# Kernel tuning notes

Measured on AMD Instinct MI355X. Metric: run time of the kernel, lower is better.

## Reference

```python
import jax, jax.numpy as jnp
import numpy as np

# 2x2 string of 4 cores at these (h, w) positions; ring bond topology.
POS = [(0, 0), (0, 1), (1, 0), (1, 1)]
MIN_H, MAX_H = 0, 1
MIN_W, MAX_W = 0, 1
STD = 0.9  # DumbNormalInitialization std


def setup_inputs() -> dict:
    key = jax.random.key(0)
    k1, k2 = jax.random.split(key)
    # channels: first dim = in_num_channels (2), each [B, H, W, in_quantum]
    channels = jax.random.normal(k1, (2, 8, 128, 128, 4), dtype=jnp.float32)
    # cores: [n_cores, out_quantum, bond_left, bond_right, in_q0, in_q1]
    cores = STD * jax.random.normal(k2, (4, 2, 8, 8, 4, 4), dtype=jnp.float32)
    return {"channels": channels, "cores": cores}


def reference(channels, cores):
    ch0, ch1 = channels[0], channels[1]  # each [B, H, W, Qin]
    inters = []
    for i in range(4):
        # First stage: contract core's in_quantum dims with both channels per pixel
        # -> [B, out_q, H, W, bond_l, bond_r]
        t = jnp.einsum('qlrij,bhwi,bhwj->bqhwlr', cores[i], ch0, ch1)
        h, w = POS[i]
        pad_top = MAX_H - MIN_H - (h - MIN_H)
        pad_bot = h - MIN_H
        pad_left = MAX_W - MIN_W - (w - MIN_W)
        pad_right = w - MIN_W
        # pad spatial dims with value 1.0 (multiplicative identity)
        t = jnp.pad(
            t,
            ((0, 0), (0, 0), (pad_top, pad_bot), (pad_left, pad_right), (0, 0), (0, 0)),
            constant_values=1.0,
        )
        inters.append(t)
    # Second stage: ring contraction over bond dims (i->j->k->l->i)
    out = jnp.einsum('bphwij,bqhwjk,brhwkl,bshwli->bhwpqrs', *inters)
    B, Hp, Wp = out.shape[:3]
    out = out.reshape(B, Hp, Wp, -1)  # merge out_quantum dims
    dh = MAX_H - MIN_H
    dw = MAX_W - MIN_W
    return out[:, dh:Hp - dh, dw:Wp - dw, :]
```

## Files before the change

kernel.cpp:

```cpp
#include <hip/hip_runtime.h>


typedef __fp16 h2 __attribute__((ext_vector_type(2)));
typedef __fp16 h4 __attribute__((ext_vector_type(4)));
typedef float  f4 __attribute__((ext_vector_type(4)));

#define NB 8
#define NH 128
#define NW 128
#define HO 127
#define WO 127
#define CH1_OFF (NB*NH*NW*4)
#define PXSTR 648
#define ZOFF  640
#define CDROW 68
#define CDSTR 544
#define SS    20

#define PIN() asm volatile("" ::: "memory")
#define PKRTZ(a, b) __builtin_amdgcn_cvt_pkrtz((a), (b))

__device__ __forceinline__ f4 mfma16(h4 a, h4 b, f4 c) {
  return __builtin_amdgcn_mfma_f32_16x16x16f16(a, b, c, 0, 0, 0);
}

__global__ __launch_bounds__(64, 3)
void convsbs_fused(const float* __restrict__ ch,
                   const float* __restrict__ cores,
                   float* __restrict__ out) {
  const int lane = threadIdx.x & 63;
  const int quad = lane >> 4;
  const int nn   = lane & 15;
  const int x8   = lane & 7;
  const f4 F4Z = {0.f, 0.f, 0.f, 0.f};

  __shared__ __align__(16) __fp16 tbuf[8 * PXSTR];
  __shared__ __align__(16) __fp16 cdb[4 * CDSTR];
  __shared__ __align__(16) float  sbuf[4 * SS];

  if (lane < 8) *(h4*)(tbuf + lane * PXSTR + ZOFF) = (h4){0, 0, 0, 0};
  PIN();

  __fp16* wrbase = tbuf + nn * PXSTR + quad * 4;
  const bool wr = (nn < 8);

  h4 wf[4][8];
#pragma unroll
  for (int c = 0; c < 4; ++c)
#pragma unroll
    for (int bi = 0; bi < 8; ++bi) {
      const int rowIdx = bi * 16 + nn;
      const int q  = rowIdx >> 6;
      const int ua = (rowIdx >> 3) & 7;
      const int ub = rowIdx & 7;
      const int l = (c & 1) ? ub : ua;
      const int r = (c & 1) ? ua : ub;
      const float4 wv = *(const float4*)(
          cores + ((((c * 2 + q) * 8 + l) * 8 + r) << 4) + quad * 4);
      h2 p0 = PKRTZ(wv.x, wv.y), p1 = PKRTZ(wv.z, wv.w);
      wf[c][bi] = (h4){p0[0], p0[1], p1[0], p1[1]};
    }

  const int hq = nn >> 3, hb = nn & 7;
  const int ctA = (quad < 2) ? ((2 + hq) * 80 + hb * 8 + quad * 4) : ZOFF;
  const int ctB = (quad < 2) ? ( hq      * 80 + hb * 8 + quad * 4) : ZOFF;
  const int dA  = (quad < 2) ? ((4 + hq) * 80 + hb * 8 + quad * 4) : ZOFF;
  const int dB  = (quad < 2) ? ((6 + hq) * 80 + hb * 8 + quad * 4) : ZOFF;
  const int ctW = (hq * 2 + (quad >> 1)) * CDROW + hb * 8 + (quad & 1) * 4;
  const int dW  = (4 + (quad >> 1) * 2 + hq) * CDROW + hb * 8 + (quad & 1) * 4;
  const int eA  = (nn >> 2) * CDSTR + (nn & 3) * CDROW + quad * 4;
  const int eB  = (nn >> 2) * CDSTR + (4 + (nn & 3)) * CDROW + quad * 4;
  const bool sW = ((nn >> 2) == quad);
  const int sWo = quad * SS + (nn & 3) * 4;
  const int sRo = quad * SS + (nn & 3) * 4 + (nn >> 2);

  const int blk = blockIdx.x;
  const int by  = blk >> 2;
  const int b   = by / 127;
  const int y   = by - b * 127;
  const int xq  = (blk & 3) * 32;
  const float* rowbase = ch + (size_t)((b * NH + y) * NW) * 4;
  float* obase = out + (size_t)((b * HO + y) * WO) * 16;

  float  a0[2][4];
  float4 a1[2][4];
  auto loadch = [&](int xtile, int bufi) {
#pragma unroll
    for (int c = 0; c < 4; ++c) {
      int col = xtile + x8 + (c & 1);
      col = col > 127 ? 127 : col;
      const float* cp = rowbase + (((c >> 1) * NW) + col) * 4;
      a0[bufi][c] = cp[quad];
      a1[bufi][c] = *(const float4*)(cp + CH1_OFF);
    }
  };

  loadch(xq, 0);

#pragma unroll
  for (int t = 0; t < 4; ++t) {
    const int cb = t & 1;

    h4 bf[4];
#pragma unroll
    for (int c = 0; c < 4; ++c) {
      const float s = a0[cb][c];
      const float4 v = a1[cb][c];
      h2 p0 = PKRTZ(s * v.x, s * v.y), p1 = PKRTZ(s * v.z, s * v.w);
      bf[c] = (h4){p0[0], p0[1], p1[0], p1[1]};
    }
    if (t < 3) loadch(xq + (t + 1) * 8, cb ^ 1);

#pragma unroll
    for (int c = 0; c < 4; ++c)
#pragma unroll
      for (int bi = 0; bi < 8; ++bi) {
        f4 acc = mfma16(wf[c][bi], bf[c], F4Z);
        h2 p0 = PKRTZ(acc[0], acc[1]), p1 = PKRTZ(acc[2], acc[3]);
        if (wr)
          *(h4*)(wrbase + c * 160 + bi * 16 + (bi >= 4 ? 16 : 0)) =
              (h4){p0[0], p0[1], p1[0], p1[1]};
      }
    PIN();

#pragma unroll
    for (int g = 0; g < 2; ++g) {
#pragma unroll
      for (int p4 = 0; p4 < 4; ++p4) {
        const __fp16* slot = tbuf + (g * 4 + p4) * PXSTR;
        __fp16* cd = cdb + p4 * CDSTR;
        h4 a1f = *(const h4*)(slot + ctA);
        h4 b1f = *(const h4*)(slot + ctB);
        f4 c0 = mfma16(a1f, b1f, F4Z);
        h2 u0 = PKRTZ(c0[0], c0[1]), u1 = PKRTZ(c0[2], c0[3]);
        *(h4*)(cd + ctW) = (h4){u0[0], u0[1], u1[0], u1[1]};
        h4 a2f = *(const h4*)(slot + dA);
        h4 b2f = *(const h4*)(slot + dB);
        f4 d0 = mfma16(a2f, b2f, F4Z);
        h2 v0 = PKRTZ(d0[0], d0[1]), v1 = PKRTZ(d0[2], d0[3]);
        *(h4*)(cd + dW) = (h4){v0[0], v0[1], v1[0], v1[1]};
      }
      PIN();

      f4 e0 = F4Z, e1 = F4Z;
      {
        h4 ea0 = *(const h4*)(cdb + eA);
        h4 eb0 = *(const h4*)(cdb + eB);
        h4 ea1 = *(const h4*)(cdb + eA + 16);
        h4 eb1 = *(const h4*)(cdb + eB + 16);
        h4 ea2 = *(const h4*)(cdb + eA + 32);
        h4 eb2 = *(const h4*)(cdb + eB + 32);
        h4 ea3 = *(const h4*)(cdb + eA + 48);
        h4 eb3 = *(const h4*)(cdb + eB + 48);
        e0 = mfma16(ea0, eb0, e0); e0 = mfma16(ea2, eb2, e0);
        e1 = mfma16(ea1, eb1, e1); e1 = mfma16(ea3, eb3, e1);
      }
      const f4 e = e0 + e1;
      if (sW) *(float4*)(sbuf + sWo) = make_float4(e[0], e[1], e[2], e[3]);
      PIN();

      const float v = sbuf[sRo];
      const int x4 = xq + t * 8 + g * 4 + quad;
      if (x4 < WO) obase[x4 * 16 + nn] = v;
      PIN();
    }
  }
}

extern "C" void kernel_launch(void* const* d_in, const int* in_sizes, int n_in,
                              void* d_out, int out_size, void* d_ws, size_t ws_size,
                              hipStream_t stream) {
  (void)in_sizes; (void)n_in; (void)d_ws; (void)ws_size; (void)out_size;
  const float* ch    = (const float*)d_in[0];
  const float* cores = (const float*)d_in[1];
  float* out = (float*)d_out;
  convsbs_fused<<<8 * 127 * 4, 64, 0, stream>>>(ch, cores, out);
}
```

Before: 95.65 us.

## Software-pipeline stage A of next tile with ring contraction of current tile

Restructures the per-tile loop so that the first-stage MFMA for the next 8-pixel tile is issued while the current tile's final ring-contraction operands are already loaded into registers. The channel prefetch is now two tiles deep. The cd buffer and sbuf are doubled so both pixel groups are processed in one pass, which removes several intermediate sync points. Launch bounds drop from 3 to 2 waves per SIMD to leave room for the extra live registers, which trades occupancy for instruction-level overlap.

New measurement: 86.52 us. -9.6%, faster.

```diff
diff --git a/kernel.cpp b/kernel.cpp
--- a/kernel.cpp
+++ b/kernel.cpp
@@ -24,7 +24,7 @@
   return __builtin_amdgcn_mfma_f32_16x16x16f16(a, b, c, 0, 0, 0);
 }
 
-__global__ __launch_bounds__(64, 3)
+__global__ __launch_bounds__(64, 2)
 void convsbs_fused(const float* __restrict__ ch,
                    const float* __restrict__ cores,
                    float* __restrict__ out) {
@@ -35,8 +35,8 @@
   const f4 F4Z = {0.f, 0.f, 0.f, 0.f};
 
   __shared__ __align__(16) __fp16 tbuf[8 * PXSTR];
-  __shared__ __align__(16) __fp16 cdb[4 * CDSTR];
-  __shared__ __align__(16) float  sbuf[4 * SS];
+  __shared__ __align__(16) __fp16 cdb[8 * CDSTR];
+  __shared__ __align__(16) float  sbuf[2][4 * SS];
 
   if (lane < 8) *(h4*)(tbuf + lane * PXSTR + ZOFF) = (h4){0, 0, 0, 0};
   PIN();
@@ -95,22 +95,15 @@
     }
   };
 
-  loadch(xq, 0);
-
-#pragma unroll
-  for (int t = 0; t < 4; ++t) {
-    const int cb = t & 1;
-
+  auto stageA = [&](int bufi) {
     h4 bf[4];
 #pragma unroll
     for (int c = 0; c < 4; ++c) {
-      const float s = a0[cb][c];
-      const float4 v = a1[cb][c];
+      const float s = a0[bufi][c];
+      const float4 v = a1[bufi][c];
       h2 p0 = PKRTZ(s * v.x, s * v.y), p1 = PKRTZ(s * v.z, s * v.w);
       bf[c] = (h4){p0[0], p0[1], p1[0], p1[1]};
     }
-    if (t < 3) loadch(xq + (t + 1) * 8, cb ^ 1);
-
 #pragma unroll
     for (int c = 0; c < 4; ++c)
 #pragma unroll
@@ -121,49 +114,68 @@
           *(h4*)(wrbase + c * 160 + bi * 16 + (bi >= 4 ? 16 : 0)) =
               (h4){p0[0], p0[1], p1[0], p1[1]};
       }
+  };
+
+  loadch(xq, 0);
+  loadch(xq + 8, 1);
+  stageA(0);
+  PIN();
+
+#pragma unroll
+  for (int t = 0; t < 4; ++t) {
+#pragma unroll
+    for (int p8 = 0; p8 < 8; ++p8) {
+      const __fp16* slot = tbuf + p8 * PXSTR;
+      __fp16* cd = cdb + p8 * CDSTR;
+      h4 a1f = *(const h4*)(slot + ctA);
+      h4 b1f = *(const h4*)(slot + ctB);
+      f4 c0 = mfma16(a1f, b1f, F4Z);
+      h2 u0 = PKRTZ(c0[0], c0[1]), u1 = PKRTZ(c0[2], c0[3]);
+      *(h4*)(cd + ctW) = (h4){u0[0], u0[1], u1[0], u1[1]};
+      h4 a2f = *(const h4*)(slot + dA);
+      h4 b2f = *(const h4*)(slot + dB);
+      f4 d0 = mfma16(a2f, b2f, F4Z);
+      h2 v0 = PKRTZ(d0[0], d0[1]), v1 = PKRTZ(d0[2], d0[3]);
+      *(h4*)(cd + dW) = (h4){v0[0], v0[1], v1[0], v1[1]};
+    }
+    PIN();
+
+    h4 ea[2][4], eb[2][4];
+#pragma unroll
+    for (int g = 0; g < 2; ++g) {
+      const __fp16* cdg = cdb + g * 4 * CDSTR;
+#pragma unroll
+      for (int kb = 0; kb < 4; ++kb) {
+        ea[g][kb] = *(const h4*)(cdg + eA + kb * 16);
+        eb[g][kb] = *(const h4*)(cdg + eB + kb * 16);
+      }
+    }
+
+    if (t < 3) {
+      stageA((t + 1) & 1);
+      if (t < 2) loadch(xq + (t + 2) * 8, t & 1);
+    }
+
+    f4 ev[2];
+#pragma unroll
+    for (int g = 0; g < 2; ++g) {
+      f4 e0 = mfma16(ea[g][0], eb[g][0], F4Z);
+      f4 e1 = mfma16(ea[g][1], eb[g][1], F4Z);
+      e0 = mfma16(ea[g][2], eb[g][2], e0);
+      e1 = mfma16(ea[g][3], eb[g][3], e1);
+      ev[g] = e0 + e1;
+      if (sW) *(float4*)(sbuf[g] + sWo) =
+          make_float4(ev[g][0], ev[g][1], ev[g][2], ev[g][3]);
+    }
     PIN();
 
 #pragma unroll
     for (int g = 0; g < 2; ++g) {
-#pragma unroll
-      for (int p4 = 0; p4 < 4; ++p4) {
-        const __fp16* slot = tbuf + (g * 4 + p4) * PXSTR;
-        __fp16* cd = cdb + p4 * CDSTR;
-        h4 a1f = *(const h4*)(slot + ctA);
-        h4 b1f = *(const h4*)(slot + ctB);
-        f4 c0 = mfma16(a1f, b1f, F4Z);
-        h2 u0 = PKRTZ(c0[0], c0[1]), u1 = PKRTZ(c0[2], c0[3]);
-        *(h4*)(cd + ctW) = (h4){u0[0], u0[1], u1[0], u1[1]};
-        h4 a2f = *(const h4*)(slot + dA);
-        h4 b2f = *(const h4*)(slot + dB);
-        f4 d0 = mfma16(a2f, b2f, F4Z);
-        h2 v0 = PKRTZ(d0[0], d0[1]), v1 = PKRTZ(d0[2], d0[3]);
-        *(h4*)(cd + dW) = (h4){v0[0], v0[1], v1[0], v1[1]};
-      }
-      PIN();
-
-      f4 e0 = F4Z, e1 = F4Z;
-      {
-        h4 ea0 = *(const h4*)(cdb + eA);
-        h4 eb0 = *(const h4*)(cdb + eB);
-        h4 ea1 = *(const h4*)(cdb + eA + 16);
-        h4 eb1 = *(const h4*)(cdb + eB + 16);
-        h4 ea2 = *(const h4*)(cdb + eA + 32);
-        h4 eb2 = *(const h4*)(cdb + eB + 32);
-        h4 ea3 = *(const h4*)(cdb + eA + 48);
-        h4 eb3 = *(const h4*)(cdb + eB + 48);
-        e0 = mfma16(ea0, eb0, e0); e0 = mfma16(ea2, eb2, e0);
-        e1 = mfma16(ea1, eb1, e1); e1 = mfma16(ea3, eb3, e1);
-      }
-      const f4 e = e0 + e1;
-      if (sW) *(float4*)(sbuf + sWo) = make_float4(e[0], e[1], e[2], e[3]);
-      PIN();
-
-      const float v = sbuf[sRo];
+      const float v = sbuf[g][sRo];
       const int x4 = xq + t * 8 + g * 4 + quad;
       if (x4 < WO) obase[x4 * 16 + nn] = v;
-      PIN();
     }
+    PIN();
   }
 }
 
```

## Software-pipeline stage A and ring contraction over 4-pixel tiles with halved LDS

Applied to the files above, without the earlier changes.

Splits the per-block work into 8 iterations of 4 output pixels and overlaps them: the next tile's first-stage MFMAs and global loads run while the current tile's final contraction happens. The pixel staging buffer shrinks to 4 slots, and launch bounds go up to 4 waves per SIMD to allow more occupancy. The loop is now rolled (unroll 1), which adds loop overhead, and the smaller stage-A tile leaves more lanes idle on the LDS writes.

After: 138.2 us. 1.44x slower.

```diff
diff --git a/kernel.cpp b/kernel.cpp
--- a/kernel.cpp
+++ b/kernel.cpp
@@ -24,25 +24,24 @@
   return __builtin_amdgcn_mfma_f32_16x16x16f16(a, b, c, 0, 0, 0);
 }
 
-__global__ __launch_bounds__(64, 3)
+__global__ __launch_bounds__(64, 4)
 void convsbs_fused(const float* __restrict__ ch,
                    const float* __restrict__ cores,
                    float* __restrict__ out) {
   const int lane = threadIdx.x & 63;
   const int quad = lane >> 4;
   const int nn   = lane & 15;
-  const int x8   = lane & 7;
   const f4 F4Z = {0.f, 0.f, 0.f, 0.f};
 
-  __shared__ __align__(16) __fp16 tbuf[8 * PXSTR];
+  __shared__ __align__(16) __fp16 tbuf[4 * PXSTR];
   __shared__ __align__(16) __fp16 cdb[4 * CDSTR];
   __shared__ __align__(16) float  sbuf[4 * SS];
 
-  if (lane < 8) *(h4*)(tbuf + lane * PXSTR + ZOFF) = (h4){0, 0, 0, 0};
+  if (lane < 4) *(h4*)(tbuf + lane * PXSTR + ZOFF) = (h4){0, 0, 0, 0};
   PIN();
 
   __fp16* wrbase = tbuf + nn * PXSTR + quad * 4;
-  const bool wr = (nn < 8);
+  const bool wr = (nn < 4);
 
   h4 wf[4][8];
 #pragma unroll
@@ -87,7 +86,7 @@
   auto loadch = [&](int xtile, int bufi) {
 #pragma unroll
     for (int c = 0; c < 4; ++c) {
-      int col = xtile + x8 + (c & 1);
+      int col = xtile + (nn & 3) + (c & 1);
       col = col > 127 ? 127 : col;
       const float* cp = rowbase + (((c >> 1) * NW) + col) * 4;
       a0[bufi][c] = cp[quad];
@@ -95,22 +94,15 @@
     }
   };
 
-  loadch(xq, 0);
-
-#pragma unroll
-  for (int t = 0; t < 4; ++t) {
-    const int cb = t & 1;
-
+  auto stageA = [&](int bufi) {
     h4 bf[4];
 #pragma unroll
     for (int c = 0; c < 4; ++c) {
-      const float s = a0[cb][c];
-      const float4 v = a1[cb][c];
+      const float s = a0[bufi][c];
+      const float4 v = a1[bufi][c];
       h2 p0 = PKRTZ(s * v.x, s * v.y), p1 = PKRTZ(s * v.z, s * v.w);
       bf[c] = (h4){p0[0], p0[1], p1[0], p1[1]};
     }
-    if (t < 3) loadch(xq + (t + 1) * 8, cb ^ 1);
-
 #pragma unroll
     for (int c = 0; c < 4; ++c)
 #pragma unroll
@@ -121,49 +113,65 @@
           *(h4*)(wrbase + c * 160 + bi * 16 + (bi >= 4 ? 16 : 0)) =
               (h4){p0[0], p0[1], p1[0], p1[1]};
       }
+  };
+
+  auto stageB = [&]() {
+#pragma unroll
+    for (int p4 = 0; p4 < 4; ++p4) {
+      const __fp16* slot = tbuf + p4 * PXSTR;
+      __fp16* cd = cdb + p4 * CDSTR;
+      h4 a1f = *(const h4*)(slot + ctA);
+      h4 b1f = *(const h4*)(slot + ctB);
+      f4 c0 = mfma16(a1f, b1f, F4Z);
+      h2 u0 = PKRTZ(c0[0], c0[1]), u1 = PKRTZ(c0[2], c0[3]);
+      *(h4*)(cd + ctW) = (h4){u0[0], u0[1], u1[0], u1[1]};
+      h4 a2f = *(const h4*)(slot + dA);
+      h4 b2f = *(const h4*)(slot + dB);
+      f4 d0 = mfma16(a2f, b2f, F4Z);
+      h2 v0 = PKRTZ(d0[0], d0[1]), v1 = PKRTZ(d0[2], d0[3]);
+      *(h4*)(cd + dW) = (h4){v0[0], v0[1], v1[0], v1[1]};
+    }
+  };
+
+  loadch(xq, 0);
+  stageA(0);
+  loadch(xq + 4, 1);
+  PIN();
+  stageB();
+  PIN();
+
+#pragma unroll 1
+  for (int k = 0; k < 8; ++k) {
+    h4 ea[4], eb[4];
+#pragma unroll
+    for (int kb = 0; kb < 4; ++kb) {
+      ea[kb] = *(const h4*)(cdb + eA + kb * 16);
+      eb[kb] = *(const h4*)(cdb + eB + kb * 16);
+    }
     PIN();
 
-#pragma unroll
-    for (int g = 0; g < 2; ++g) {
-#pragma unroll
-      for (int p4 = 0; p4 < 4; ++p4) {
-        const __fp16* slot = tbuf + (g * 4 + p4) * PXSTR;
-        __fp16* cd = cdb + p4 * CDSTR;
-        h4 a1f = *(const h4*)(slot + ctA);
-        h4 b1f = *(const h4*)(slot + ctB);
-        f4 c0 = mfma16(a1f, b1f, F4Z);
-        h2 u0 = PKRTZ(c0[0], c0[1]), u1 = PKRTZ(c0[2], c0[3]);
-        *(h4*)(cd + ctW) = (h4){u0[0], u0[1], u1[0], u1[1]};
-        h4 a2f = *(const h4*)(slot + dA);
-        h4 b2f = *(const h4*)(slot + dB);
-        f4 d0 = mfma16(a2f, b2f, F4Z);
-        h2 v0 = PKRTZ(d0[0], d0[1]), v1 = PKRTZ(d0[2], d0[3]);
-        *(h4*)(cd + dW) = (h4){v0[0], v0[1], v1[0], v1[1]};
-      }
-      PIN();
+    if (k < 7) {
+      stageA((k + 1) & 1);
+      if (k < 6) loadch(xq + (k + 2) * 4, k & 1);
+    }
+    PIN();
 
-      f4 e0 = F4Z, e1 = F4Z;
-      {
-        h4 ea0 = *(const h4*)(cdb + eA);
-        h4 eb0 = *(const h4*)(cdb + eB);
-        h4 ea1 = *(const h4*)(cdb + eA + 16);
-        h4 eb1 = *(const h4*)(cdb + eB + 16);
-        h4 ea2 = *(const h4*)(cdb + eA + 32);
-        h4 eb2 = *(const h4*)(cdb + eB + 32);
-        h4 ea3 = *(const h4*)(cdb + eA + 48);
-        h4 eb3 = *(const h4*)(cdb + eB + 48);
-        e0 = mfma16(ea0, eb0, e0); e0 = mfma16(ea2, eb2, e0);
-        e1 = mfma16(ea1, eb1, e1); e1 = mfma16(ea3, eb3, e1);
-      }
-      const f4 e = e0 + e1;
-      if (sW) *(float4*)(sbuf + sWo) = make_float4(e[0], e[1], e[2], e[3]);
-      PIN();
+    f4 e0 = mfma16(ea[0], eb[0], F4Z);
+    f4 e1 = mfma16(ea[1], eb[1], F4Z);
+    e0 = mfma16(ea[2], eb[2], e0);
+    e1 = mfma16(ea[3], eb[3], e1);
+    const f4 e = e0 + e1;
+    if (sW) *(float4*)(sbuf + sWo) = make_float4(e[0], e[1], e[2], e[3]);
+    PIN();
+    {
+      const float v = sbuf[sRo];
+      const int x4 = xq + k * 4 + quad;
+      if (x4 < WO) obase[x4 * 16 + nn] = v;
+    }
+    PIN();
 
-      const float v = sbuf[sRo];
-      const int x4 = xq + t * 8 + g * 4 + quad;
-      if (x4 < WO) obase[x4 * 16 + nn] = v;
-      PIN();
-    }
+    if (k < 7) stageB();
+    PIN();
   }
 }
 
```
